# Kernel tuning notes

Hardware: AMD Instinct MI355X
Metric: run time of the kernel (lower is better)

The kernel has to match this reference:

```python
import jax, jax.numpy as jnp
import numpy as np
from jax import lax

B, N, CIN, H, W = 1, 6, 256, 32, 88
COUT = 80
IMG_H, IMG_W = 256, 704
XB = (-51.2, 51.2, 0.8); YB = (-51.2, 51.2, 0.8); ZB = (-5.0, 3.0, 0.8)
NX, NY, NZ = 128, 128, 10
EPS = 1e-5


def _voxel_coords(b0, b1, vs):
    n = int(round((b1 - b0) / vs))
    return jnp.linspace(b0 + 0.5 * vs, b1 - 0.5 * vs, n, dtype=jnp.float32)


def _make_points():
    xs = _voxel_coords(*XB); ys = _voxel_coords(*YB); zs = _voxel_coords(*ZB)
    gx, gy, gz = jnp.meshgrid(xs, ys, zs, indexing='ij')
    return jnp.stack([gx, gy, gz], -1).reshape(-1, 3)  # [M,3], M = NX*NY*NZ


def _conv(x, w, b=None, pad=1):
    y = lax.conv_general_dilated(x, w, (1, 1), [(pad, pad), (pad, pad)],
                                 dimension_numbers=('NCHW', 'OIHW', 'NCHW'))
    if b is not None:
        y = y + b[None, :, None, None]
    return y


def _bn(x, g, b, m, v):
    return (g[None, :, None, None] * (x - m[None, :, None, None])
            * lax.rsqrt(v[None, :, None, None] + EPS) + b[None, :, None, None])


def _bilinear(feat, gx, gy):
    # feat [C,Hf,Wf]; gx,gy [M] in [-1,1]; align_corners=True, zero padding
    C, Hf, Wf = feat.shape
    ix = (gx + 1.0) * 0.5 * (Wf - 1)
    iy = (gy + 1.0) * 0.5 * (Hf - 1)
    ix0 = jnp.floor(ix); iy0 = jnp.floor(iy)
    wx1 = ix - ix0; wy1 = iy - iy0

    def tap(iyf, ixf, wgt):
        valid = (ixf >= 0) & (ixf < Wf) & (iyf >= 0) & (iyf < Hf)
        ii = jnp.clip(ixf, 0, Wf - 1).astype(jnp.int32)
        jj = jnp.clip(iyf, 0, Hf - 1).astype(jnp.int32)
        return feat[:, jj, ii] * (wgt * valid)[None, :]

    return (tap(iy0, ix0, (1 - wy1) * (1 - wx1))
            + tap(iy0, ix0 + 1, (1 - wy1) * wx1)
            + tap(iy0 + 1, ix0, wy1 * (1 - wx1))
            + tap(iy0 + 1, ix0 + 1, wy1 * wx1))


def reference(img, lidar2image, w1, b1, g1, beta1, m1, v1,
              w2, b2, g2, beta2, m2, v2, w3, b3):
    # proj_net: conv3x3+BN+ReLU, conv3x3+BN+ReLU, conv1x1
    x = img.reshape(B * N, CIN, H, W)
    x = jax.nn.relu(_bn(_conv(x, w1, b1), g1, beta1, m1, v1))
    x = jax.nn.relu(_bn(_conv(x, w2, b2), g2, beta2, m2, v2))
    feat = _conv(x, w3, b3, pad=0)  # [B*N, COUT, H, W]

    pts = _make_points()  # [M,3]
    R = lidar2image[:, :, :3, :3].reshape(B * N, 3, 3)
    t = lidar2image[:, :, :3, 3].reshape(B * N, 3, 1)
    proj = jnp.einsum('kij,mj->kim', R, pts) + t  # [BN,3,M]
    dist = proj[:, 2]
    px = proj[:, 0] / dist
    py = proj[:, 1] / dist
    gx = px / IMG_W * 2.0 - 1.0
    gy = py / IMG_H * 2.0 - 1.0

    sampled = jax.vmap(_bilinear)(feat, gx, gy)  # [BN, COUT, M]
    on_img = (px < IMG_W) & (px > 0) & (py < IMG_H) & (py > 0) & (dist > 0.1)
    sampled = jnp.where(on_img[:, None, :], sampled, 0.0)

    vox = sampled.reshape(B, N, COUT, NX, NY, NZ)
    bev = jnp.max(vox, axis=1).mean(axis=-1)  # [B, COUT, NX, NY]
    return bev


def setup_inputs() -> dict:
    key = jax.random.key(0)
    ks = jax.random.split(key, 8)
    img = jax.random.normal(ks[0], (B, N, CIN, H, W), jnp.float32)

    # Plausible lidar->image matrices: 6 cameras in a ring, pinhole intrinsics.
    fx = fy = 280.0; cx = IMG_W / 2.0; cy = IMG_H / 2.0
    K = np.array([[fx, 0.0, cx], [0.0, fy, cy], [0.0, 0.0, 1.0]])
    mats = []
    for k in range(N):
        th = 2.0 * np.pi * k / N
        fwd = np.array([np.cos(th), np.sin(th), 0.0])
        rgt = np.array([np.sin(th), -np.cos(th), 0.0])
        dwn = np.array([0.0, 0.0, -1.0])
        Rm = np.stack([rgt, dwn, fwd], 0)
        c = np.array([0.5 * np.cos(th), 0.5 * np.sin(th), 1.5])
        M4 = np.eye(4)
        M4[:3, :3] = K @ Rm
        M4[:3, 3] = K @ (-Rm @ c)
        mats.append(M4)
    lidar2image = jnp.asarray(np.broadcast_to(np.stack(mats), (B, N, 4, 4)).copy(),
                              jnp.float32)

    def w(k, shape, s=0.02):
        return jax.random.normal(k, shape, jnp.float32) * s

    zc = lambda c: jnp.zeros((c,), jnp.float32)
    oc = lambda c: jnp.ones((c,), jnp.float32)
    return dict(
        img=img, lidar2image=lidar2image,
        w1=w(ks[1], (CIN, CIN, 3, 3)), b1=zc(CIN),
        g1=oc(CIN), beta1=zc(CIN), m1=zc(CIN), v1=oc(CIN),
        w2=w(ks[2], (CIN, CIN, 3, 3)), b2=zc(CIN),
        g2=oc(CIN), beta2=zc(CIN), m2=zc(CIN), v2=oc(CIN),
        w3=w(ks[3], (COUT, CIN, 1, 1)), b3=zc(COUT),
    )
```

## Files before the change

kernel.cpp:

```cpp
#include <hip/hip_runtime.h>
#include <math.h>

#define N_IMG 6
#define CIN   256
#define H_IN  32
#define W_IN  88
#define SP    2816
#define HH    34
#define WW    90
#define SPH   3060
#define COUTC 80
#define EPSBN 1e-5f

typedef _Float16 half8 __attribute__((ext_vector_type(8)));
typedef _Float16 half2v __attribute__((ext_vector_type(2)));
typedef float floatx4 __attribute__((ext_vector_type(4)));

#define AS1 __attribute__((address_space(1)))
#define AS3 __attribute__((address_space(3)))

__global__ __launch_bounds__(256) void prep_w33(const float* __restrict__ wa,
                                                const float* __restrict__ wb,
                                                _Float16* __restrict__ wTa,
                                                _Float16* __restrict__ wTb) {
  __shared__ float s[2304];
  const int oc = blockIdx.x;
  const int tid = threadIdx.x;
  const float* w = blockIdx.y ? wb : wa;
  _Float16* wT = blockIdx.y ? wTb : wTa;
  const float* wo = w + (size_t)oc * 2304;
  for (int i = tid; i < 2304; i += 256) s[i] = wo[i];
  __syncthreads();
  for (int i = tid; i < 2304; i += 256) {
    const int tap = i >> 8;
    const int ic  = i & 255;
    wT[((size_t)tap * 256 + oc) * 256 + ic] = (_Float16)s[ic * 9 + tap];
  }
}

__global__ __launch_bounds__(256) void prep_misc(const float* __restrict__ w3,
                                                 _Float16* __restrict__ wT3,
                                                 _Float16* __restrict__ a,
                                                 _Float16* __restrict__ b) {
  const int bx = blockIdx.x;
  const int tid = threadIdx.x;
  if (bx < 80) {
    const int idx = bx * 256 + tid;
    wT3[idx] = (_Float16)w3[idx];
  } else {
    const int im = bx - 80;
    for (int s = tid; s < 244 * 32; s += 256) {
      const int pos = s >> 5;
      const int gr  = s & 31;
      int h, w;
      if (pos < 90)       { h = 0;  w = pos; }
      else if (pos < 180) { h = 33; w = pos - 90; }
      else { const int r = pos - 180; h = 1 + (r >> 1); w = (r & 1) * 89; }
      const size_t off = ((size_t)im * SPH + h * WW + w) * CIN + gr * 8;
      half8 z = {};
      *(half8*)(a + off) = z;
      *(half8*)(b + off) = z;
    }
  }
}

__global__ __launch_bounds__(256) void nchw_to_nhwc(const float* __restrict__ img,
                                                    _Float16* __restrict__ x0) {
  __shared__ float t[64][65];
  const int sp0 = blockIdx.x * 64;
  const int ic0 = blockIdx.y * 64;
  const int im  = blockIdx.z;
  const int tx = threadIdx.x & 63;
  const int ty = threadIdx.x >> 6;
  for (int r = ty; r < 64; r += 4)
    t[r][tx] = img[((size_t)(im * CIN + ic0 + r)) * SP + sp0 + tx];
  __syncthreads();
  for (int r = ty; r < 64; r += 4) {
    const int sp = sp0 + r;
    const int h = sp / 88;
    const int w = sp - h * 88;
    x0[((size_t)im * SPH + h * WW + w + WW + 1) * CIN + ic0 + tx] = (_Float16)t[tx][r];
  }
}

__global__ __launch_bounds__(256) void conv3x3_mfma(
    const _Float16* __restrict__ x, const _Float16* __restrict__ wT,
    const float* __restrict__ bias, const float* __restrict__ gamma,
    const float* __restrict__ beta, const float* __restrict__ bnm,
    const float* __restrict__ bnv, _Float16* __restrict__ out,
    int OW, int OB, int imStride)
{
  __shared__ _Float16 As[2][128 * 64];
  __shared__ _Float16 Bs[2][128 * 64];

  const int tid  = threadIdx.x;
  const int wv   = tid >> 6;
  const int lane = tid & 63;
  const int m0   = blockIdx.x * 128;
  const int n0   = blockIdx.y * 128;
  const int im   = blockIdx.z;
  const _Float16* xim = x + (size_t)im * SPH * CIN;

  int srcA[4], srcB[4];
  #pragma unroll
  for (int i = 0; i < 4; ++i) {
    const int g = i * 256 + wv * 64 + lane;
    const int row = g >> 3;
    const int lg  = (g & 7) ^ (row & 7);
    const int m = m0 + row;
    const int h = m / 88;
    const int w = m - h * 88;
    srcA[i] = ((h + 1) * WW + (w + 1)) * CIN + lg * 8;
    srcB[i] = (n0 + row) * 256 + lg * 8;
  }

  const int fr = lane & 15;
  const int q  = lane >> 4;
  const int q4 = q * 4;
  const int mw = (wv & 1) * 64;
  const int nw = (wv >> 1) * 64;

  floatx4 acc[4][4];
  #pragma unroll
  for (int i = 0; i < 4; ++i)
    #pragma unroll
    for (int j = 0; j < 4; ++j) {
      acc[i][j][0] = 0.f; acc[i][j][1] = 0.f; acc[i][j][2] = 0.f; acc[i][j][3] = 0.f;
    }

  {
    const int aoff0 = (-1 * WW - 1) * CIN;
    #pragma unroll
    for (int i = 0; i < 4; ++i)
      __builtin_amdgcn_global_load_lds(
          (const AS1 void*)(xim + srcA[i] + aoff0),
          (AS3 void*)(&As[0][(i * 256 + wv * 64) * 8]), 16, 0, 0);
    #pragma unroll
    for (int i = 0; i < 4; ++i)
      __builtin_amdgcn_global_load_lds(
          (const AS1 void*)(wT + srcB[i]),
          (AS3 void*)(&Bs[0][(i * 256 + wv * 64) * 8]), 16, 0, 0);
  }

  for (int c = 0; c < 36; ++c) {
    __syncthreads();
    if (c < 35) {
      const int cn   = c + 1;
      const int tapn = cn >> 2;
      const int iccn = (cn & 3) << 6;
      const int dyn  = tapn / 3 - 1;
      const int dxn  = tapn - (tapn / 3) * 3 - 1;
      const int aoffn = (dyn * WW + dxn) * CIN + iccn;
      const size_t boffn = (size_t)tapn * 65536 + iccn;
      const int nb = cn & 1;
      #pragma unroll
      for (int i = 0; i < 4; ++i)
        __builtin_amdgcn_global_load_lds(
            (const AS1 void*)(xim + srcA[i] + aoffn),
            (AS3 void*)(&As[nb][(i * 256 + wv * 64) * 8]), 16, 0, 0);
      #pragma unroll
      for (int i = 0; i < 4; ++i)
        __builtin_amdgcn_global_load_lds(
            (const AS1 void*)(wT + boffn + srcB[i]),
            (AS3 void*)(&Bs[nb][(i * 256 + wv * 64) * 8]), 16, 0, 0);
    }
    const int cb = c & 1;
    #pragma unroll
    for (int ks = 0; ks < 2; ++ks) {
      half8 af[4], bf[4];
      #pragma unroll
      for (int i = 0; i < 4; ++i) {
        const int row = mw + i * 16 + fr;
        af[i] = *(const half8*)(&As[cb][row * 64 + (((ks * 4 + q) ^ (row & 7)) * 8)]);
      }
      #pragma unroll
      for (int j = 0; j < 4; ++j) {
        const int row = nw + j * 16 + fr;
        bf[j] = *(const half8*)(&Bs[cb][row * 64 + (((ks * 4 + q) ^ (row & 7)) * 8)]);
      }
      #pragma unroll
      for (int i = 0; i < 4; ++i)
        #pragma unroll
        for (int j = 0; j < 4; ++j)
          acc[i][j] = __builtin_amdgcn_mfma_f32_16x16x32_f16(af[i], bf[j], acc[i][j], 0, 0, 0);
    }
  }

  #pragma unroll
  for (int j = 0; j < 4; ++j) {
    const int oc = n0 + nw + j * 16 + fr;
    const float sc = gamma[oc] * rsqrtf(bnv[oc] + EPSBN);
    const float sh = (bias[oc] - bnm[oc]) * sc + beta[oc];
    #pragma unroll
    for (int i = 0; i < 4; ++i) {
      #pragma unroll
      for (int r = 0; r < 4; ++r) {
        const int m = m0 + mw + i * 16 + q4 + r;
        const int h = m / 88;
        const int w = m - h * 88;
        const float v = fmaxf(fmaf(acc[i][j][r], sc, sh), 0.f);
        out[((size_t)im * imStride + h * OW + w + OB) * CIN + oc] = (_Float16)v;
      }
    }
  }
}

__global__ __launch_bounds__(128) void conv1x1_mfma(
    const _Float16* __restrict__ x, const _Float16* __restrict__ wT,
    const float* __restrict__ bias, _Float16* __restrict__ feat)
{
  __shared__ _Float16 Bs[80 * 264];

  const int tid = threadIdx.x;
  const int m0  = blockIdx.x * 64;
  const int wv   = tid >> 6;
  const int lane = tid & 63;
  const int fr  = lane & 15;
  const int q8  = (lane >> 4) * 8;
  const int q4  = (lane >> 4) * 4;

  for (int g = tid; g < 2560; g += 128) {
    const int oc = g >> 5;
    const int kg8 = (g & 31) << 3;
    *(half8*)(&Bs[oc * 264 + kg8]) = *(const half8*)(wT + oc * 256 + kg8);
  }
  __syncthreads();

  floatx4 acc[2][5];
  #pragma unroll
  for (int i = 0; i < 2; ++i)
    #pragma unroll
    for (int j = 0; j < 5; ++j) {
      acc[i][j][0] = 0.f; acc[i][j][1] = 0.f; acc[i][j][2] = 0.f; acc[i][j][3] = 0.f;
    }

  const _Float16* xa = x + (size_t)(m0 + wv * 32 + fr) * 256 + q8;
  #pragma unroll
  for (int ks = 0; ks < 8; ++ks) {
    half8 af[2], bf[5];
    #pragma unroll
    for (int i = 0; i < 2; ++i)
      af[i] = *(const half8*)(xa + (size_t)i * 16 * 256 + ks * 32);
    #pragma unroll
    for (int j = 0; j < 5; ++j)
      bf[j] = *(const half8*)(&Bs[(j * 16 + fr) * 264 + ks * 32 + q8]);
    #pragma unroll
    for (int i = 0; i < 2; ++i)
      #pragma unroll
      for (int j = 0; j < 5; ++j)
        acc[i][j] = __builtin_amdgcn_mfma_f32_16x16x32_f16(af[i], bf[j], acc[i][j], 0, 0, 0);
  }

  #pragma unroll
  for (int j = 0; j < 5; ++j) {
    const int oc = j * 16 + fr;
    const float bb = bias[oc];
    #pragma unroll
    for (int i = 0; i < 2; ++i) {
      const int mbase = m0 + wv * 32 + i * 16 + q4;
      #pragma unroll
      for (int r = 0; r < 4; ++r)
        feat[(size_t)(mbase + r) * COUTC + oc] = (_Float16)(acc[i][j][r] + bb);
    }
  }
}

__global__ __launch_bounds__(320) void bev_sample(
    const _Float16* __restrict__ feat, const float* __restrict__ l2i,
    float* __restrict__ tmp)
{
  __shared__ int4   eo[480];
  __shared__ float4 ew[480];
  const int tid = threadIdx.x;
  const int cellBase = blockIdx.x * 8;

  for (int e = tid; e < 480; e += 320) {
    const int cell = e / 60;
    const int idx = e - cell * 60;
    const int n = idx / 10;
    const int z = idx - n * 10;
    const int cid = cellBase + cell;
    const int gix = cid >> 7;
    const int giy = cid & 127;
    const float X = (float)(-50.8 + (double)gix * (101.6 / 127.0));
    const float Y = (float)(-50.8 + (double)giy * (101.6 / 127.0));
    const float Z = (float)(-4.6 + (double)z * (7.2 / 9.0));
    const float* M = l2i + n * 16;
    const float pw = M[0] * X + M[1] * Y + M[2] * Z + M[3];
    const float ph = M[4] * X + M[5] * Y + M[6] * Z + M[7];
    const float d  = M[8] * X + M[9] * Y + M[10] * Z + M[11];
    const float px = pw / d;
    const float py = ph / d;
    const bool on_img = (px < 704.f) && (px > 0.f) && (py < 256.f) && (py > 0.f) && (d > 0.1f);
    const float gx = px / 704.f * 2.f - 1.f;
    const float gy = py / 256.f * 2.f - 1.f;
    const float ixf = (gx + 1.f) * 0.5f * 87.f;
    const float iyf = (gy + 1.f) * 0.5f * 31.f;
    const float ix0 = floorf(ixf);
    const float iy0 = floorf(iyf);
    const float wx1 = ixf - ix0;
    const float wy1 = iyf - iy0;
    const float ix1 = ix0 + 1.f, iy1 = iy0 + 1.f;
    float w00 = (1.f - wy1) * (1.f - wx1);
    float w01 = (1.f - wy1) * wx1;
    float w10 = wy1 * (1.f - wx1);
    float w11 = wy1 * wx1;
    const bool vx0 = (ix0 >= 0.f) && (ix0 < 88.f);
    const bool vx1 = (ix1 >= 0.f) && (ix1 < 88.f);
    const bool vy0 = (iy0 >= 0.f) && (iy0 < 32.f);
    const bool vy1 = (iy1 >= 0.f) && (iy1 < 32.f);
    if (!(on_img && vy0 && vx0)) w00 = 0.f;
    if (!(on_img && vy0 && vx1)) w01 = 0.f;
    if (!(on_img && vy1 && vx0)) w10 = 0.f;
    if (!(on_img && vy1 && vx1)) w11 = 0.f;
    const int i0 = (int)fminf(fmaxf(ix0, 0.f), 87.f);
    const int i1 = (int)fminf(fmaxf(ix1, 0.f), 87.f);
    const int j0 = (int)fminf(fmaxf(iy0, 0.f), 31.f);
    const int j1 = (int)fminf(fmaxf(iy1, 0.f), 31.f);
    const int base = n * SP;
    eo[e] = make_int4((base + j0 * 88 + i0) * COUTC,
                      (base + j0 * 88 + i1) * COUTC,
                      (base + j1 * 88 + i0) * COUTC,
                      (base + j1 * 88 + i1) * COUTC);
    ew[e] = make_float4(w00, w01, w10, w11);
  }
  __syncthreads();

  const int c2 = (tid % 40) * 2;
  const int cell = tid / 40;
  const int ebase = cell * 60;
  float a0 = 0.f, a1 = 0.f;
  for (int z = 0; z < 10; ++z) {
    float mx0 = -INFINITY, mx1 = -INFINITY;
    #pragma unroll
    for (int n = 0; n < 6; ++n) {
      const float4 w = ew[ebase + n * 10 + z];
      if (w.x + w.y + w.z + w.w > 0.f) {
        const int4 o = eo[ebase + n * 10 + z];
        const half2v p00 = *(const half2v*)(feat + o.x + c2);
        const half2v p01 = *(const half2v*)(feat + o.y + c2);
        const half2v p10 = *(const half2v*)(feat + o.z + c2);
        const half2v p11 = *(const half2v*)(feat + o.w + c2);
        float v0 = w.x * (float)p00[0];
        float v1 = w.x * (float)p00[1];
        v0 = fmaf(w.y, (float)p01[0], v0);  v1 = fmaf(w.y, (float)p01[1], v1);
        v0 = fmaf(w.z, (float)p10[0], v0);  v1 = fmaf(w.z, (float)p10[1], v1);
        v0 = fmaf(w.w, (float)p11[0], v0);  v1 = fmaf(w.w, (float)p11[1], v1);
        mx0 = fmaxf(mx0, v0);
        mx1 = fmaxf(mx1, v1);
      } else {
        mx0 = fmaxf(mx0, 0.f);
        mx1 = fmaxf(mx1, 0.f);
      }
    }
    a0 += mx0;
    a1 += mx1;
  }
  const int cid = cellBase + cell;
  float2 res = make_float2(a0 * 0.1f, a1 * 0.1f);
  *(float2*)(&tmp[(size_t)cid * COUTC + c2]) = res;
}

__global__ __launch_bounds__(256) void bev_transpose(const float* __restrict__ tmp,
                                                     float* __restrict__ out)
{
  __shared__ float tile[32][33];
  const int mBase = blockIdx.x * 32;
  const int cBase = blockIdx.y * 32;
  const int tx = threadIdx.x & 31;
  const int ty = threadIdx.x >> 5;
  for (int i = ty; i < 32; i += 8) {
    const int cc = cBase + tx;
    tile[i][tx] = (cc < COUTC) ? tmp[(size_t)(mBase + i) * COUTC + cc] : 0.f;
  }
  __syncthreads();
  for (int i = ty; i < 32; i += 8) {
    const int cc = cBase + i;
    if (cc < COUTC) out[(size_t)cc * 16384 + mBase + tx] = tile[tx][i];
  }
}

extern "C" void kernel_launch(void* const* d_in, const int* in_sizes, int n_in,
                              void* d_out, int out_size, void* d_ws, size_t ws_size,
                              hipStream_t stream)
{
  const float* img = (const float*)d_in[0];
  const float* l2i = (const float*)d_in[1];
  const float* w1  = (const float*)d_in[2];
  const float* b1  = (const float*)d_in[3];
  const float* g1  = (const float*)d_in[4];
  const float* be1 = (const float*)d_in[5];
  const float* m1  = (const float*)d_in[6];
  const float* v1  = (const float*)d_in[7];
  const float* w2  = (const float*)d_in[8];
  const float* b2  = (const float*)d_in[9];
  const float* g2  = (const float*)d_in[10];
  const float* be2 = (const float*)d_in[11];
  const float* m2  = (const float*)d_in[12];
  const float* v2  = (const float*)d_in[13];
  const float* w3  = (const float*)d_in[14];
  const float* b3  = (const float*)d_in[15];

  char* ws = (char*)d_ws;
  _Float16* wT1h = (_Float16*)ws;  ws += (size_t)9 * CIN * CIN * 2;
  _Float16* wT2h = (_Float16*)ws;  ws += (size_t)9 * CIN * CIN * 2;
  _Float16* wT3h = (_Float16*)ws;  ws += (size_t)CIN * COUTC * 2;
  _Float16* x0   = (_Float16*)ws;  ws += (size_t)N_IMG * SPH * CIN * 2;
  _Float16* x1h  = (_Float16*)ws;  ws += (size_t)N_IMG * SPH * CIN * 2;
  _Float16* x2h  = (_Float16*)ws;  ws += (size_t)N_IMG * SP * CIN * 2;
  _Float16* feat = (_Float16*)ws;  ws += (size_t)N_IMG * SP * COUTC * 2;
  float*    tmp  = (float*)ws;
  float*    outp = (float*)d_out;

  prep_misc<<<86, 256, 0, stream>>>(w3, wT3h, x0, x1h);
  prep_w33<<<dim3(256, 2), 256, 0, stream>>>(w1, w2, wT1h, wT2h);
  nchw_to_nhwc<<<dim3(44, 4, 6), 256, 0, stream>>>(img, x0);

  conv3x3_mfma<<<dim3(22, 2, 6), 256, 0, stream>>>(x0, wT1h, b1, g1, be1, m1, v1,
                                                   x1h, WW, WW + 1, SPH);
  conv3x3_mfma<<<dim3(22, 2, 6), 256, 0, stream>>>(x1h, wT2h, b2, g2, be2, m2, v2,
                                                   x2h, 88, 0, SP);
  conv1x1_mfma<<<264, 128, 0, stream>>>(x2h, wT3h, b3, feat);

  bev_sample<<<2048, 320, 0, stream>>>(feat, l2i, tmp);
  bev_transpose<<<dim3(512, 3), 256, 0, stream>>>(tmp, outp);
}
```

Measured before the change: 249.1 us.

## Shrink conv M-tile to 64 for more blocks; vectorize BEV sampling to 8 channels

```diff
diff --git a/kernel.cpp b/kernel.cpp
--- a/kernel.cpp
+++ b/kernel.cpp
@@ -13,7 +13,6 @@
 #define EPSBN 1e-5f
 
 typedef _Float16 half8 __attribute__((ext_vector_type(8)));
-typedef _Float16 half2v __attribute__((ext_vector_type(2)));
 typedef float floatx4 __attribute__((ext_vector_type(4)));
 
 #define AS1 __attribute__((address_space(1)))
@@ -90,39 +89,47 @@
     const float* __restrict__ bnv, _Float16* __restrict__ out,
     int OW, int OB, int imStride)
 {
-  __shared__ _Float16 As[2][128 * 64];
+  __shared__ _Float16 As[2][64 * 64];
   __shared__ _Float16 Bs[2][128 * 64];
 
   const int tid  = threadIdx.x;
   const int wv   = tid >> 6;
   const int lane = tid & 63;
-  const int m0   = blockIdx.x * 128;
-  const int n0   = blockIdx.y * 128;
-  const int im   = blockIdx.z;
+  const int bx   = blockIdx.x;
+  const int n0   = (bx & 1) << 7;
+  const int mt   = bx >> 1;
+  const int im   = mt / 44;
+  const int m0sp = (mt - im * 44) * 64;
   const _Float16* xim = x + (size_t)im * SPH * CIN;
 
-  int srcA[4], srcB[4];
+  int srcA[2], srcB[4];
+  #pragma unroll
+  for (int i = 0; i < 2; ++i) {
+    const int g = i * 256 + wv * 64 + lane;
+    const int row = g >> 3;
+    const int lg  = (g & 7) ^ (row & 7);
+    const int m = m0sp + row;
+    const int h = m / 88;
+    const int w = m - h * 88;
+    srcA[i] = ((h + 1) * WW + (w + 1)) * CIN + lg * 8;
+  }
   #pragma unroll
   for (int i = 0; i < 4; ++i) {
     const int g = i * 256 + wv * 64 + lane;
     const int row = g >> 3;
     const int lg  = (g & 7) ^ (row & 7);
-    const int m = m0 + row;
-    const int h = m / 88;
-    const int w = m - h * 88;
-    srcA[i] = ((h + 1) * WW + (w + 1)) * CIN + lg * 8;
     srcB[i] = (n0 + row) * 256 + lg * 8;
   }
 
   const int fr = lane & 15;
   const int q  = lane >> 4;
   const int q4 = q * 4;
-  const int mw = (wv & 1) * 64;
+  const int mw = (wv & 1) * 32;
   const int nw = (wv >> 1) * 64;
 
-  floatx4 acc[4][4];
-  #pragma unroll
-  for (int i = 0; i < 4; ++i)
+  floatx4 acc[2][4];
+  #pragma unroll
+  for (int i = 0; i < 2; ++i)
     #pragma unroll
     for (int j = 0; j < 4; ++j) {
       acc[i][j][0] = 0.f; acc[i][j][1] = 0.f; acc[i][j][2] = 0.f; acc[i][j][3] = 0.f;
@@ -131,7 +138,7 @@
   {
     const int aoff0 = (-1 * WW - 1) * CIN;
     #pragma unroll
-    for (int i = 0; i < 4; ++i)
+    for (int i = 0; i < 2; ++i)
       __builtin_amdgcn_global_load_lds(
           (const AS1 void*)(xim + srcA[i] + aoff0),
           (AS3 void*)(&As[0][(i * 256 + wv * 64) * 8]), 16, 0, 0);
@@ -154,7 +161,7 @@
       const size_t boffn = (size_t)tapn * 65536 + iccn;
       const int nb = cn & 1;
       #pragma unroll
-      for (int i = 0; i < 4; ++i)
+      for (int i = 0; i < 2; ++i)
         __builtin_amdgcn_global_load_lds(
             (const AS1 void*)(xim + srcA[i] + aoffn),
             (AS3 void*)(&As[nb][(i * 256 + wv * 64) * 8]), 16, 0, 0);
@@ -167,9 +174,9 @@
     const int cb = c & 1;
     #pragma unroll
     for (int ks = 0; ks < 2; ++ks) {
-      half8 af[4], bf[4];
-      #pragma unroll
-      for (int i = 0; i < 4; ++i) {
+      half8 af[2], bf[4];
+      #pragma unroll
+      for (int i = 0; i < 2; ++i) {
         const int row = mw + i * 16 + fr;
         af[i] = *(const half8*)(&As[cb][row * 64 + (((ks * 4 + q) ^ (row & 7)) * 8)]);
       }
@@ -179,7 +186,7 @@
         bf[j] = *(const half8*)(&Bs[cb][row * 64 + (((ks * 4 + q) ^ (row & 7)) * 8)]);
       }
       #pragma unroll
-      for (int i = 0; i < 4; ++i)
+      for (int i = 0; i < 2; ++i)
         #pragma unroll
         for (int j = 0; j < 4; ++j)
           acc[i][j] = __builtin_amdgcn_mfma_f32_16x16x32_f16(af[i], bf[j], acc[i][j], 0, 0, 0);
@@ -192,10 +199,10 @@
     const float sc = gamma[oc] * rsqrtf(bnv[oc] + EPSBN);
     const float sh = (bias[oc] - bnm[oc]) * sc + beta[oc];
     #pragma unroll
-    for (int i = 0; i < 4; ++i) {
+    for (int i = 0; i < 2; ++i) {
       #pragma unroll
       for (int r = 0; r < 4; ++r) {
-        const int m = m0 + mw + i * 16 + q4 + r;
+        const int m = m0sp + mw + i * 16 + q4 + r;
         const int h = m / 88;
         const int w = m - h * 88;
         const float v = fmaxf(fmaf(acc[i][j][r], sc, sh), 0.f);
@@ -269,12 +276,12 @@
     const _Float16* __restrict__ feat, const float* __restrict__ l2i,
     float* __restrict__ tmp)
 {
-  __shared__ int4   eo[480];
-  __shared__ float4 ew[480];
+  __shared__ int4   eo[1920];
+  __shared__ float4 ew[1920];
   const int tid = threadIdx.x;
-  const int cellBase = blockIdx.x * 8;
-
-  for (int e = tid; e < 480; e += 320) {
+  const int cellBase = blockIdx.x * 32;
+
+  for (int e = tid; e < 1920; e += 320) {
     const int cell = e / 60;
     const int idx = e - cell * 60;
     const int n = idx / 10;
@@ -326,39 +333,47 @@
   }
   __syncthreads();
 
-  const int c2 = (tid % 40) * 2;
-  const int cell = tid / 40;
+  const int grp  = tid % 10;
+  const int c8   = grp * 8;
+  const int cell = tid / 10;
   const int ebase = cell * 60;
-  float a0 = 0.f, a1 = 0.f;
+  float acc[8];
+  #pragma unroll
+  for (int k = 0; k < 8; ++k) acc[k] = 0.f;
+
   for (int z = 0; z < 10; ++z) {
-    float mx0 = -INFINITY, mx1 = -INFINITY;
+    float mx[8];
+    #pragma unroll
+    for (int k = 0; k < 8; ++k) mx[k] = -INFINITY;
     #pragma unroll
     for (int n = 0; n < 6; ++n) {
       const float4 w = ew[ebase + n * 10 + z];
       if (w.x + w.y + w.z + w.w > 0.f) {
         const int4 o = eo[ebase + n * 10 + z];
-        const half2v p00 = *(const half2v*)(feat + o.x + c2);
-        const half2v p01 = *(const half2v*)(feat + o.y + c2);
-        const half2v p10 = *(const half2v*)(feat + o.z + c2);
-        const half2v p11 = *(const half2v*)(feat + o.w + c2);
-        float v0 = w.x * (float)p00[0];
-        float v1 = w.x * (float)p00[1];
-        v0 = fmaf(w.y, (float)p01[0], v0);  v1 = fmaf(w.y, (float)p01[1], v1);
-        v0 = fmaf(w.z, (float)p10[0], v0);  v1 = fmaf(w.z, (float)p10[1], v1);
-        v0 = fmaf(w.w, (float)p11[0], v0);  v1 = fmaf(w.w, (float)p11[1], v1);
-        mx0 = fmaxf(mx0, v0);
-        mx1 = fmaxf(mx1, v1);
+        const half8 p00 = *(const half8*)(feat + o.x + c8);
+        const half8 p01 = *(const half8*)(feat + o.y + c8);
+        const half8 p10 = *(const half8*)(feat + o.z + c8);
+        const half8 p11 = *(const half8*)(feat + o.w + c8);
+        #pragma unroll
+        for (int k = 0; k < 8; ++k) {
+          float v = w.x * (float)p00[k];
+          v = fmaf(w.y, (float)p01[k], v);
+          v = fmaf(w.z, (float)p10[k], v);
+          v = fmaf(w.w, (float)p11[k], v);
+          mx[k] = fmaxf(mx[k], v);
+        }
       } else {
-        mx0 = fmaxf(mx0, 0.f);
-        mx1 = fmaxf(mx1, 0.f);
+        #pragma unroll
+        for (int k = 0; k < 8; ++k) mx[k] = fmaxf(mx[k], 0.f);
       }
     }
-    a0 += mx0;
-    a1 += mx1;
+    #pragma unroll
+    for (int k = 0; k < 8; ++k) acc[k] += mx[k];
   }
   const int cid = cellBase + cell;
-  float2 res = make_float2(a0 * 0.1f, a1 * 0.1f);
-  *(float2*)(&tmp[(size_t)cid * COUTC + c2]) = res;
+  float* op = tmp + (size_t)cid * COUTC + c8;
+  #pragma unroll
+  for (int k = 0; k < 8; ++k) op[k] = acc[k] * 0.1f;
 }
 
 __global__ __launch_bounds__(256) void bev_transpose(const float* __restrict__ tmp,
@@ -416,12 +431,12 @@
   prep_w33<<<dim3(256, 2), 256, 0, stream>>>(w1, w2, wT1h, wT2h);
   nchw_to_nhwc<<<dim3(44, 4, 6), 256, 0, stream>>>(img, x0);
 
-  conv3x3_mfma<<<dim3(22, 2, 6), 256, 0, stream>>>(x0, wT1h, b1, g1, be1, m1, v1,
-                                                   x1h, WW, WW + 1, SPH);
-  conv3x3_mfma<<<dim3(22, 2, 6), 256, 0, stream>>>(x1h, wT2h, b2, g2, be2, m2, v2,
-                                                   x2h, 88, 0, SP);
+  conv3x3_mfma<<<528, 256, 0, stream>>>(x0, wT1h, b1, g1, be1, m1, v1,
+                                        x1h, WW, WW + 1, SPH);
+  conv3x3_mfma<<<528, 256, 0, stream>>>(x1h, wT2h, b2, g2, be2, m2, v2,
+                                        x2h, 88, 0, SP);
   conv1x1_mfma<<<264, 128, 0, stream>>>(x2h, wT3h, b3, feat);
 
-  bev_sample<<<2048, 320, 0, stream>>>(feat, l2i, tmp);
+  bev_sample<<<512, 320, 0, stream>>>(feat, l2i, tmp);
   bev_transpose<<<dim3(512, 3), 256, 0, stream>>>(tmp, outp);
 }
```

After: 221.9 us. 10.9% less time.
